# Optimization experiments

Measured on AMD Instinct MI355X. Metric: run time of the kernel, lower is better.

The kernel has to match this reference:

```python
import jax, jax.numpy as jnp
import numpy as np

RADIUS = 1.0
NORM_ORD = 2.0
N_POINTS = 4194304


def _contract(p):
    # p: [..., 3] -> contracted points [..., 3] (MipNeRF-360 eq. 10)
    eps = jnp.finfo(p.dtype).eps
    mag = jnp.linalg.norm(p, ord=NORM_ORD, axis=-1)
    mag = jnp.maximum(mag, eps)
    norm_factor = (2.0 - RADIUS / mag) / mag
    mask = (mag <= RADIUS)[..., None]
    return jnp.where(mask, p / RADIUS, norm_factor[..., None] * p)


def setup_inputs() -> dict:
    key = jax.random.key(0)
    x = jax.random.normal(key, (N_POINTS, 3), dtype=jnp.float32) * 2.0
    return {"x": x, "output_jacobian": 1}


def reference(x, output_jacobian):
    x_contr = _contract(x)
    if output_jacobian:
        # per-point 3x3 jacobian, mirroring torch.func.vmap(jacrev(contract))
        jacobian = jax.vmap(jax.jacrev(_contract))(x.reshape(-1, x.shape[-1]))
        jacobian = jacobian.reshape(x.shape[:-1] + (x.shape[-1], x.shape[-1]))
        return (x_contr, jacobian)
    return x_contr
```

## Files before the change

kernel.cpp:

```cpp
#include <hip/hip_runtime.h>


constexpr int BLOCK = 256;
constexpr int PPB   = 1024;

__global__ __launch_bounds__(BLOCK) void contract_jac_kernel(
    const float* __restrict__ x,
    float* __restrict__ out,
    long long n_points)
{
    __shared__ float4 sbuf[PPB * 9 / 4];

    const int tid = threadIdx.x;
    float* sw = reinterpret_cast<float*>(sbuf);

    const float4* x4 = reinterpret_cast<const float4*>(x) + (long long)blockIdx.x * 768;
    #pragma unroll
    for (int i = 0; i < 3; ++i)
        sbuf[tid + i * BLOCK] = x4[tid + i * BLOCK];
    __syncthreads();

    float oc[12];
    float oj[36];
    #pragma unroll
    for (int k = 0; k < 4; ++k) {
        const int j = tid + k * BLOCK;
        float px = sw[j * 3 + 0];
        float py = sw[j * 3 + 1];
        float pz = sw[j * 3 + 2];

        float m2 = fmaf(px, px, fmaf(py, py, pz * pz));
        float m  = sqrtf(m2);

        float s, coef;
        if (m <= 1.0f) {
            s = 1.0f;
            coef = 0.0f;
        } else {
            float inv = 1.0f / m;
            s = (2.0f - inv) * inv;
            coef = 2.0f * (1.0f - m) / (m2 * m2);
        }

        oc[k * 3 + 0] = s * px;
        oc[k * 3 + 1] = s * py;
        oc[k * 3 + 2] = s * pz;

        float cx = coef * px, cy = coef * py, cz = coef * pz;
        oj[k * 9 + 0] = fmaf(cx, px, s);
        oj[k * 9 + 1] = cx * py;
        oj[k * 9 + 2] = cx * pz;
        oj[k * 9 + 3] = cy * px;
        oj[k * 9 + 4] = fmaf(cy, py, s);
        oj[k * 9 + 5] = cy * pz;
        oj[k * 9 + 6] = cz * px;
        oj[k * 9 + 7] = cz * py;
        oj[k * 9 + 8] = fmaf(cz, pz, s);
    }
    __syncthreads();

    #pragma unroll
    for (int k = 0; k < 4; ++k) {
        const int j = tid + k * BLOCK;
        sw[j * 3 + 0] = oc[k * 3 + 0];
        sw[j * 3 + 1] = oc[k * 3 + 1];
        sw[j * 3 + 2] = oc[k * 3 + 2];
    }
    __syncthreads();
    float4* oc4 = reinterpret_cast<float4*>(out) + (long long)blockIdx.x * 768;
    #pragma unroll
    for (int i = 0; i < 3; ++i)
        oc4[tid + i * BLOCK] = sbuf[tid + i * BLOCK];
    __syncthreads();

    #pragma unroll
    for (int k = 0; k < 4; ++k) {
        const int j = tid + k * BLOCK;
        #pragma unroll
        for (int c = 0; c < 9; ++c)
            sw[j * 9 + c] = oj[k * 9 + c];
    }
    __syncthreads();
    float4* oj4 = reinterpret_cast<float4*>(out + n_points * 3) + (long long)blockIdx.x * 2304;
    #pragma unroll
    for (int i = 0; i < 9; ++i)
        oj4[tid + i * BLOCK] = sbuf[tid + i * BLOCK];
}

extern "C" void kernel_launch(void* const* d_in, const int* in_sizes, int n_in,
                              void* d_out, int out_size, void* d_ws, size_t ws_size,
                              hipStream_t stream) {
    const float* x = (const float*)d_in[0];
    float* out = (float*)d_out;

    long long n = in_sizes[0] / 3;
    int grid = (int)(n / PPB);

    contract_jac_kernel<<<grid, BLOCK, 0, stream>>>(x, out, n);
}
```

Baseline: 239.3 us.

## Recompute outputs from shared scalars and use nontemporal vector stores

Each point now stores only its input coordinates and two scalars (s, coef) in shared memory. Output threads then rebuild the contracted point and the Jacobian entries directly in coalesced float4 order, using index arithmetic. This drops the register staging and the extra shared-memory round trips and barriers, and cuts LDS use from 36KB to 20KB, which may allow more resident blocks. The final writes use nontemporal stores to avoid cache pollution. The cost is extra integer division and recomputation plus scattered LDS reads that may hit bank conflicts.

```diff
diff --git a/kernel.cpp b/kernel.cpp
--- a/kernel.cpp
+++ b/kernel.cpp
@@ -1,5 +1,7 @@
 #include <hip/hip_runtime.h>
 
+
+typedef float v4f __attribute__((ext_vector_type(4)));
 
 constexpr int BLOCK = 256;
 constexpr int PPB   = 1024;
@@ -9,82 +11,68 @@
     float* __restrict__ out,
     long long n_points)
 {
-    __shared__ float4 sbuf[PPB * 9 / 4];
+    __shared__ float  sp[PPB * 3];
+    __shared__ float2 ssc[PPB];
 
     const int tid = threadIdx.x;
-    float* sw = reinterpret_cast<float*>(sbuf);
+    const long long blk = blockIdx.x;
 
-    const float4* x4 = reinterpret_cast<const float4*>(x) + (long long)blockIdx.x * 768;
+    const v4f* x4 = reinterpret_cast<const v4f*>(x) + blk * 768;
+    v4f* sp4 = reinterpret_cast<v4f*>(sp);
     #pragma unroll
     for (int i = 0; i < 3; ++i)
-        sbuf[tid + i * BLOCK] = x4[tid + i * BLOCK];
-    __syncthreads();
-
-    float oc[12];
-    float oj[36];
-    #pragma unroll
-    for (int k = 0; k < 4; ++k) {
-        const int j = tid + k * BLOCK;
-        float px = sw[j * 3 + 0];
-        float py = sw[j * 3 + 1];
-        float pz = sw[j * 3 + 2];
-
-        float m2 = fmaf(px, px, fmaf(py, py, pz * pz));
-        float m  = sqrtf(m2);
-
-        float s, coef;
-        if (m <= 1.0f) {
-            s = 1.0f;
-            coef = 0.0f;
-        } else {
-            float inv = 1.0f / m;
-            s = (2.0f - inv) * inv;
-            coef = 2.0f * (1.0f - m) / (m2 * m2);
-        }
-
-        oc[k * 3 + 0] = s * px;
-        oc[k * 3 + 1] = s * py;
-        oc[k * 3 + 2] = s * pz;
-
-        float cx = coef * px, cy = coef * py, cz = coef * pz;
-        oj[k * 9 + 0] = fmaf(cx, px, s);
-        oj[k * 9 + 1] = cx * py;
-        oj[k * 9 + 2] = cx * pz;
-        oj[k * 9 + 3] = cy * px;
-        oj[k * 9 + 4] = fmaf(cy, py, s);
-        oj[k * 9 + 5] = cy * pz;
-        oj[k * 9 + 6] = cz * px;
-        oj[k * 9 + 7] = cz * py;
-        oj[k * 9 + 8] = fmaf(cz, pz, s);
-    }
+        sp4[tid + i * BLOCK] = x4[tid + i * BLOCK];
     __syncthreads();
 
     #pragma unroll
     for (int k = 0; k < 4; ++k) {
-        const int j = tid + k * BLOCK;
-        sw[j * 3 + 0] = oc[k * 3 + 0];
-        sw[j * 3 + 1] = oc[k * 3 + 1];
-        sw[j * 3 + 2] = oc[k * 3 + 2];
+        int q = tid + k * BLOCK;
+        float px = sp[3*q + 0], py = sp[3*q + 1], pz = sp[3*q + 2];
+        float m2 = fmaf(px, px, fmaf(py, py, pz * pz));
+        float m  = sqrtf(m2);
+        float s = 1.0f, coef = 0.0f;
+        if (m > 1.0f) {
+            float inv = 1.0f / m;
+            s    = (2.0f - inv) * inv;
+            coef = 2.0f * (1.0f - m) / (m2 * m2);
+        }
+        ssc[q] = make_float2(s, coef);
     }
     __syncthreads();
-    float4* oc4 = reinterpret_cast<float4*>(out) + (long long)blockIdx.x * 768;
+
+    float* ocb = out + blk * 3072;
     #pragma unroll
-    for (int i = 0; i < 3; ++i)
-        oc4[tid + i * BLOCK] = sbuf[tid + i * BLOCK];
-    __syncthreads();
+    for (int i = 0; i < 3; ++i) {
+        int g = tid + i * BLOCK;
+        v4f v;
+        #pragma unroll
+        for (int j = 0; j < 4; ++j) {
+            unsigned F = 4u * g + j;
+            unsigned q = F / 3u;
+            v[j] = ssc[q].x * sp[F];
+        }
+        __builtin_nontemporal_store(v, reinterpret_cast<v4f*>(ocb) + g);
+    }
 
+    float* ojb = out + n_points * 3 + blk * 9216;
     #pragma unroll
-    for (int k = 0; k < 4; ++k) {
-        const int j = tid + k * BLOCK;
+    for (int i = 0; i < 9; ++i) {
+        int g = tid + i * BLOCK;
+        v4f v;
         #pragma unroll
-        for (int c = 0; c < 9; ++c)
-            sw[j * 9 + c] = oj[k * 9 + c];
+        for (int j = 0; j < 4; ++j) {
+            unsigned E = 4u * g + j;
+            unsigned q = E / 9u;
+            unsigned r = E - 9u * q;
+            unsigned a = (r * 11u) >> 5;
+            unsigned b = r - 3u * a;
+            float2 sc2 = ssc[q];
+            float val = sc2.y * sp[3u*q + a] * sp[3u*q + b];
+            val = (a == b) ? val + sc2.x : val;
+            v[j] = val;
+        }
+        __builtin_nontemporal_store(v, reinterpret_cast<v4f*>(ojb) + g);
     }
-    __syncthreads();
-    float4* oj4 = reinterpret_cast<float4*>(out + n_points * 3) + (long long)blockIdx.x * 2304;
-    #pragma unroll
-    for (int i = 0; i < 9; ++i)
-        oj4[tid + i * BLOCK] = sbuf[tid + i * BLOCK];
 }
 
 extern "C" void kernel_launch(void* const* d_in, const int* in_sizes, int n_in,
```

Result: no change. 239.2 us (-0.0%).
